# Optimization experiments

Hardware: AMD Instinct MI355X
Metric: run time of the kernel (lower is better)

The kernel has to match this reference:

```python
import jax, jax.numpy as jnp
import numpy as np

EPS = 1e-8


def setup_inputs() -> dict:
    key = jax.random.key(0)
    k1, k2 = jax.random.split(key)
    N, F, K, C = 16384, 64, 32, 100
    membership = jax.random.uniform(k1, (N, F, K), dtype=jnp.float32)
    teacher_probs = jax.random.uniform(k2, (N, C), dtype=jnp.float32)
    return {"membership": membership, "teacher_probs": teacher_probs}


def reference(membership, teacher_probs):
    # membership: [N, F, K]  soft bin assignments per feature
    # teacher_probs: [N, C]  teacher class distribution per sample
    N, F, K = membership.shape
    bin_mass = membership.sum(axis=0) + EPS  # [F, K]
    # Contraction form of (membership[:, :, :, None] * teacher_probs[:, None, None, :]).sum(0)
    # avoids the N*F*K*C intermediate.
    centroids = jnp.einsum('nfk,nc->fkc', membership, teacher_probs) / bin_mass[:, :, None]  # [F, K, C]
    # Intra-bin: minimize entropy of each bin's class distribution, mass-weighted.
    intra_entropy = -jnp.sum(centroids * jnp.log(centroids + EPS), axis=2)  # [F, K]
    loss_intra = jnp.sum(intra_entropy * bin_mass) / N
    # Inter-bin: maximize entropy of the mixture of adjacent bins
    # (loss_inter is negative entropy summed, added with +0.5 weight).
    mixture = 0.5 * (centroids[:, :-1, :] + centroids[:, 1:, :])  # [F, K-1, C]
    loss_inter = jnp.sum(mixture * jnp.log(mixture + EPS))
    return loss_intra + 0.5 * loss_inter
```

## Files before the change

### kernel.cpp

```cpp
#include <hip/hip_runtime.h>
#include <hip/hip_bf16.h>

#define NS   16384
#define FKD  2048
#define CD   100
#define CP   112
#define MT   64
#define NKC  32
#define PHASES 16
#define EPSF 1e-8f
#define SFK  (FKD * CP)
#define NGRP (NS / 8)

typedef float f32x4 __attribute__((ext_vector_type(4)));
typedef short bf16x8 __attribute__((ext_vector_type(8)));

__device__ inline unsigned short f2bf(float f) {
    unsigned int u = __float_as_uint(f);
    u += 0x7FFFu + ((u >> 16) & 1u);
    return (unsigned short)(u >> 16);
}

__device__ __forceinline__ void gload4(const float* g, const float* l) {
    __builtin_amdgcn_global_load_lds(
        (const __attribute__((address_space(1))) void*)g,
        (__attribute__((address_space(3))) void*)l, 4, 0, 0);
}

__global__ __launch_bounds__(256) void ebl_prep(
    const float* __restrict__ tp, unsigned short* __restrict__ Bp)
{
    const int idx = blockIdx.x * 256 + threadIdx.x;
    if (idx >= NGRP * CP) return;
    const int g = idx / CP, c = idx - g * CP;
    unsigned short v[8];
    if (c < CD) {
        const float* p = tp + (size_t)g * 8 * CD + c;
        #pragma unroll
        for (int j = 0; j < 8; ++j) v[j] = f2bf(p[(size_t)j * CD]);
    } else {
        const unsigned short fill = (c == CD) ? 0x3F80 : 0;
        #pragma unroll
        for (int j = 0; j < 8; ++j) v[j] = fill;
    }
    *reinterpret_cast<uint4*>(Bp + (size_t)idx * 8) = *reinterpret_cast<const uint4*>(v);
}

__global__ __launch_bounds__(256) void ebl_gemm(
    const float* __restrict__ mem, const unsigned short* __restrict__ Bp,
    unsigned short* __restrict__ spart)
{
    __shared__ float At[3 * 4 * 8 * 68];

    const int t  = threadIdx.x;
    const int w  = t >> 6;
    const int l  = t & 63;
    const int lg = l >> 4, lr = l & 15;
    const int m0 = blockIdx.x * MT;
    const int kc = blockIdx.y;
    const int n0 = kc * (PHASES * 32);
    const int gb = n0 >> 3;

    const float* gbase = mem + (size_t)(n0 + lg) * FKD + (m0 + w * 16 + lr);

    f32x4 acc[7];
    #pragma unroll
    for (int i = 0; i < 7; ++i) acc[i] = (f32x4){0.f, 0.f, 0.f, 0.f};

    bf16x8 b0[7], b1[7];
    int o0 = (0 * 4 + w) * 544, o1 = (1 * 4 + w) * 544, o2 = (2 * 4 + w) * 544;

#define SB() __builtin_amdgcn_sched_barrier(0)
#define STAGE(bo, p) { \
    const float* gs = gbase + (size_t)(p) * 32 * FKD; \
    _Pragma("unroll") \
    for (int q = 0; q < 8; ++q) \
        gload4(gs + (size_t)q * 4 * FKD, At + (bo) + q * 68); \
    SB(); }
#define LOADB(dst, p) { \
    const unsigned short* bq = Bp + ((size_t)(gb + (p) * 4 + lg) * CP + lr) * 8; \
    _Pragma("unroll") \
    for (int nt = 0; nt < 7; ++nt) dst[nt] = *reinterpret_cast<const bf16x8*>(bq + nt * 128); \
    SB(); }
#define WAITV(n) { asm volatile("s_waitcnt vmcnt(" #n ")" ::: "memory"); SB(); }
#define COMPUTE(bo, bB) { \
    bf16x8 af; \
    _Pragma("unroll") \
    for (int j = 0; j < 8; ++j) { \
        float v = At[(bo) + (2 * lg + (j >> 2)) * 68 + (j & 3) * 16 + lr]; \
        af[j] = (short)f2bf(v); } \
    _Pragma("unroll") \
    for (int nt = 0; nt < 7; ++nt) \
        acc[nt] = __builtin_amdgcn_mfma_f32_16x16x32_bf16(af, bB[nt], acc[nt], 0, 0, 0); }

    STAGE(o0, 0)
    LOADB(b0, 0)
    STAGE(o1, 1)

    for (int ph = 0; ph < PHASES - 2; ph += 2) {
        LOADB(b1, ph + 1)
        STAGE(o2, ph + 2)
        WAITV(23)
        COMPUTE(o0, b0)
        LOADB(b0, ph + 2)
        STAGE(o0, ph + 3)
        WAITV(23)
        COMPUTE(o1, b1)
        const int tmp = o2; o2 = o1; o1 = o0; o0 = tmp;
    }
    LOADB(b1, PHASES - 1)
    WAITV(15)
    COMPUTE(o0, b0)
    WAITV(0)
    COMPUTE(o1, b1)

#undef SB
#undef STAGE
#undef LOADB
#undef WAITV
#undef COMPUTE

    unsigned short* sp = spart + (size_t)kc * SFK;
    #pragma unroll
    for (int nt = 0; nt < 7; ++nt) {
        const int c = nt * 16 + lr;
        #pragma unroll
        for (int r = 0; r < 4; ++r) {
            const int mm = m0 + w * 16 + lg * 4 + r;
            sp[(size_t)mm * CP + c] = f2bf(acc[nt][r]);
        }
    }
}

__global__ __launch_bounds__(256) void ebl_reduce(
    const unsigned short* __restrict__ spart, float* __restrict__ S)
{
    const int idx = blockIdx.x * 256 + threadIdx.x;
    if (idx >= SFK / 2) return;
    float s0 = 0.f, s1 = 0.f;
    for (int p = 0; p < NKC; ++p) {
        const unsigned raw = *reinterpret_cast<const unsigned*>(spart + (size_t)p * SFK + (size_t)idx * 2);
        s0 += __uint_as_float(raw << 16);
        s1 += __uint_as_float(raw & 0xFFFF0000u);
    }
    *reinterpret_cast<float2*>(S + (size_t)idx * 2) = make_float2(s0, s1);
}

__global__ __launch_bounds__(256) void ebl_entropy(
    const float* __restrict__ S, float* __restrict__ fpart)
{
    __shared__ float Ss[32 * CP];
    __shared__ float massL[32];
    __shared__ float red[4];
    const int t = threadIdx.x;
    const int f = blockIdx.x;

    for (int idx = t; idx < 32 * CP; idx += 256)
        Ss[idx] = S[(size_t)f * 32 * CP + idx];
    __syncthreads();
    if (t < 32) massL[t] = Ss[t * CP + CD] + EPSF;
    __syncthreads();

    float a_int = 0.f, a_mix = 0.f;
    for (int idx = t; idx < 32 * CD; idx += 256) {
        const int k = idx / CD, c = idx - k * CD;
        const float cent = Ss[k * CP + c] / massL[k];
        a_int -= cent * logf(cent + EPSF) * massL[k];
    }
    for (int idx = t; idx < 31 * CD; idx += 256) {
        const int k = idx / CD, c = idx - k * CD;
        const float mix = 0.5f * (Ss[k * CP + c] / massL[k] + Ss[(k + 1) * CP + c] / massL[k + 1]);
        a_mix += mix * logf(mix + EPSF);
    }

    float part = a_int * (1.0f / (float)NS) + 0.5f * a_mix;
    #pragma unroll
    for (int off = 32; off > 0; off >>= 1) part += __shfl_down(part, off);
    if ((t & 63) == 0) red[t >> 6] = part;
    __syncthreads();
    if (t == 0) fpart[f] = (red[0] + red[1]) + (red[2] + red[3]);
}

__global__ void ebl_finalize(const float* __restrict__ fpart, float* __restrict__ out) {
    float v = fpart[threadIdx.x];
    #pragma unroll
    for (int off = 32; off > 0; off >>= 1) v += __shfl_down(v, off);
    if (threadIdx.x == 0) out[0] = v;
}

extern "C" void kernel_launch(void* const* d_in, const int* in_sizes, int n_in,
                              void* d_out, int out_size, void* d_ws, size_t ws_size,
                              hipStream_t stream)
{
    const float* mem = (const float*)d_in[0];
    const float* tp  = (const float*)d_in[1];
    float* out = (float*)d_out;

    const size_t bpBytes = (size_t)NGRP * CP * 8 * 2;

    unsigned short* Bp    = (unsigned short*)d_ws;
    unsigned short* spart = (unsigned short*)((char*)d_ws + bpBytes);
    float*          S     = (float*)((char*)spart + (size_t)NKC * SFK * 2);
    float*          fpart = S + SFK;

    ebl_prep<<<(NGRP * CP + 255) / 256, 256, 0, stream>>>(tp, Bp);
    dim3 grid(FKD / MT, NKC);
    ebl_gemm<<<grid, 256, 0, stream>>>(mem, Bp, spart);
    ebl_reduce<<<(SFK / 2 + 255) / 256, 256, 0, stream>>>(spart, S);
    ebl_entropy<<<64, 256, 0, stream>>>(S, fpart);
    ebl_finalize<<<1, 64, 0, stream>>>(fpart, out);
}
```

Before: 55.52 us.

## Widen GEMM tile per wave to four M-subtiles with 16-byte LDS-direct loads

Each wave now computes four 16-row M subtiles instead of one, so each B fragment loaded from global is reused across four MFMA rows and B traffic per output drops. The global-to-LDS staging switches from 4-byte to 16-byte global_load_lds, cutting the number of load instructions. Blocks shrink to 128 threads covering 128 M rows, halving the grid. The cost is four times the accumulator registers per thread (28 f32x4), which may reduce occupancy. LDS reads may also hit bank conflicts now that the padded layout is gone.

After: 51.48 us (median of 2 runs). -7.3%, faster.

```diff
diff --git a/kernel.cpp b/kernel.cpp
--- a/kernel.cpp
+++ b/kernel.cpp
@@ -5,7 +5,6 @@
 #define FKD  2048
 #define CD   100
 #define CP   112
-#define MT   64
 #define NKC  32
 #define PHASES 16
 #define EPSF 1e-8f
@@ -21,10 +20,10 @@
     return (unsigned short)(u >> 16);
 }
 
-__device__ __forceinline__ void gload4(const float* g, const float* l) {
+__device__ __forceinline__ void gload16(const float* g, const float* l) {
     __builtin_amdgcn_global_load_lds(
         (const __attribute__((address_space(1))) void*)g,
-        (__attribute__((address_space(3))) void*)l, 4, 0, 0);
+        (__attribute__((address_space(3))) void*)l, 16, 0, 0);
 }
 
 __global__ __launch_bounds__(256) void ebl_prep(
@@ -46,36 +45,38 @@
     *reinterpret_cast<uint4*>(Bp + (size_t)idx * 8) = *reinterpret_cast<const uint4*>(v);
 }
 
-__global__ __launch_bounds__(256) void ebl_gemm(
+__global__ __launch_bounds__(128) void ebl_gemm(
     const float* __restrict__ mem, const unsigned short* __restrict__ Bp,
     unsigned short* __restrict__ spart)
 {
-    __shared__ float At[3 * 4 * 8 * 68];
+    __shared__ float At[3 * 2 * 2048];
 
     const int t  = threadIdx.x;
     const int w  = t >> 6;
     const int l  = t & 63;
     const int lg = l >> 4, lr = l & 15;
-    const int m0 = blockIdx.x * MT;
+    const int m0 = blockIdx.x * 128;
     const int kc = blockIdx.y;
     const int n0 = kc * (PHASES * 32);
     const int gb = n0 >> 3;
 
-    const float* gbase = mem + (size_t)(n0 + lg) * FKD + (m0 + w * 16 + lr);
-
-    f32x4 acc[7];
-    #pragma unroll
-    for (int i = 0; i < 7; ++i) acc[i] = (f32x4){0.f, 0.f, 0.f, 0.f};
+    const float* gbase = mem + (size_t)(n0 + lg) * FKD + (m0 + w * 64 + lr * 4);
+
+    f32x4 acc[4][7];
+    #pragma unroll
+    for (int i = 0; i < 4; ++i)
+        #pragma unroll
+        for (int nt = 0; nt < 7; ++nt) acc[i][nt] = (f32x4){0.f, 0.f, 0.f, 0.f};
 
     bf16x8 b0[7], b1[7];
-    int o0 = (0 * 4 + w) * 544, o1 = (1 * 4 + w) * 544, o2 = (2 * 4 + w) * 544;
+    int o0 = (0 * 2 + w) * 2048, o1 = (1 * 2 + w) * 2048, o2 = (2 * 2 + w) * 2048;
 
 #define SB() __builtin_amdgcn_sched_barrier(0)
 #define STAGE(bo, p) { \
     const float* gs = gbase + (size_t)(p) * 32 * FKD; \
     _Pragma("unroll") \
     for (int q = 0; q < 8; ++q) \
-        gload4(gs + (size_t)q * 4 * FKD, At + (bo) + q * 68); \
+        gload16(gs + (size_t)q * 4 * FKD, At + (bo) + q * 256); \
     SB(); }
 #define LOADB(dst, p) { \
     const unsigned short* bq = Bp + ((size_t)(gb + (p) * 4 + lg) * CP + lr) * 8; \
@@ -84,14 +85,18 @@
     SB(); }
 #define WAITV(n) { asm volatile("s_waitcnt vmcnt(" #n ")" ::: "memory"); SB(); }
 #define COMPUTE(bo, bB) { \
-    bf16x8 af; \
-    _Pragma("unroll") \
-    for (int j = 0; j < 8; ++j) { \
-        float v = At[(bo) + (2 * lg + (j >> 2)) * 68 + (j & 3) * 16 + lr]; \
-        af[j] = (short)f2bf(v); } \
-    _Pragma("unroll") \
-    for (int nt = 0; nt < 7; ++nt) \
-        acc[nt] = __builtin_amdgcn_mfma_f32_16x16x32_bf16(af, bB[nt], acc[nt], 0, 0, 0); }
+    bf16x8 af[4]; \
+    _Pragma("unroll") \
+    for (int i = 0; i < 4; ++i) \
+        _Pragma("unroll") \
+        for (int j = 0; j < 8; ++j) { \
+            float v = At[(bo) + (2 * lg + (j >> 2)) * 256 + (j & 3) * 64 + i * 16 + lr]; \
+            af[i][j] = (short)f2bf(v); } \
+    _Pragma("unroll") \
+    for (int i = 0; i < 4; ++i) \
+        _Pragma("unroll") \
+        for (int nt = 0; nt < 7; ++nt) \
+            acc[i][nt] = __builtin_amdgcn_mfma_f32_16x16x32_bf16(af[i], bB[nt], acc[i][nt], 0, 0, 0); }
 
     STAGE(o0, 0)
     LOADB(b0, 0)
@@ -122,12 +127,15 @@
 
     unsigned short* sp = spart + (size_t)kc * SFK;
     #pragma unroll
-    for (int nt = 0; nt < 7; ++nt) {
-        const int c = nt * 16 + lr;
-        #pragma unroll
-        for (int r = 0; r < 4; ++r) {
-            const int mm = m0 + w * 16 + lg * 4 + r;
-            sp[(size_t)mm * CP + c] = f2bf(acc[nt][r]);
+    for (int i = 0; i < 4; ++i) {
+        #pragma unroll
+        for (int nt = 0; nt < 7; ++nt) {
+            const int c = nt * 16 + lr;
+            #pragma unroll
+            for (int r = 0; r < 4; ++r) {
+                const int mm = m0 + w * 64 + i * 16 + lg * 4 + r;
+                sp[(size_t)mm * CP + c] = f2bf(acc[i][nt][r]);
+            }
         }
     }
 }
@@ -204,8 +212,8 @@
     float*          fpart = S + SFK;
 
     ebl_prep<<<(NGRP * CP + 255) / 256, 256, 0, stream>>>(tp, Bp);
-    dim3 grid(FKD / MT, NKC);
-    ebl_gemm<<<grid, 256, 0, stream>>>(mem, Bp, spart);
+    dim3 grid(FKD / 128, NKC);
+    ebl_gemm<<<grid, 128, 0, stream>>>(mem, Bp, spart);
     ebl_reduce<<<(SFK / 2 + 255) / 256, 256, 0, stream>>>(spart, S);
     ebl_entropy<<<64, 256, 0, stream>>>(S, fpart);
     ebl_finalize<<<1, 64, 0, stream>>>(fpart, out);
```
